# Kernel optimization log

Hardware: AMD Instinct MI355X
Metric: run time of the kernel (lower is better)

The kernel has to match this reference:

```python
import jax, jax.numpy as jnp
import numpy as np

B, N, FIN, FOUT = 32, 1024, 128, 128
NEG_SLOPE = 0.01  # torch nn.LeakyReLU default


def setup_inputs() -> dict:
    key = jax.random.key(0)
    k1, k2, k3, k4 = jax.random.split(key, 4)
    node_mat = jax.random.normal(k1, (B, N, FIN), dtype=jnp.float32)
    adj_mat = jax.random.uniform(k2, (B, N, N), dtype=jnp.float32)
    # nn.Linear(FIN, FOUT): weight [FOUT, FIN], bias [FOUT]
    bound = 1.0 / np.sqrt(FIN)
    W = jax.random.uniform(k3, (FOUT, FIN), minval=-bound, maxval=bound, dtype=jnp.float32)
    b = jax.random.uniform(k4, (FOUT,), minval=-bound, maxval=bound, dtype=jnp.float32)
    return {"node_mat": node_mat, "adj_mat": adj_mat, "W": W, "b": b}


def reference(node_mat, adj_mat, W, b):
    # degree per node: row-sum of adjacency [B, N, 1]
    n_neighbors = adj_mat.sum(axis=-1, keepdims=True)
    # D^-1 A : the original builds eye*(1/deg) then bmm; algebraically a row scaling
    norm_adj = adj_mat / n_neighbors                      # [B, N, N]
    agg = jnp.einsum('bnm,bmf->bnf', norm_adj, node_mat)  # [B, N, FIN]
    out = jnp.einsum('bnf,of->bno', agg, W) + b           # [B, N, FOUT]
    return jnp.where(out >= 0, out, NEG_SLOPE * out)      # LeakyReLU
```

## Files before the change

kernel.cpp:

```cpp
#include <hip/hip_runtime.h>
#include <cstdint>
#include <cstddef>

#define BB   32
#define NN   1024
#define FIN  128
#define FOUT 128

typedef __attribute__((ext_vector_type(8))) short bf16x8;
typedef __attribute__((ext_vector_type(4))) float f32x4;

__device__ __forceinline__ unsigned int f2bf(float f) {
    union { float f; unsigned int u; } v; v.f = f;
    unsigned int u = v.u;
    return (u + 0x7FFFu + ((u >> 16) & 1u)) >> 16;
}
__device__ __forceinline__ unsigned int pack2(float a, float b) {
    return f2bf(a) | (f2bf(b) << 16);
}

__global__ __launch_bounds__(256) void y_kernel(const float* __restrict__ node,
                                                const float* __restrict__ W,
                                                unsigned short* __restrict__ Yt) {
    __shared__ unsigned short Alds[64 * 136];
    __shared__ unsigned short Blds[128 * 136];

    const int tid = threadIdx.x;
    const int bid = blockIdx.x;
    const int b   = bid >> 4;
    const int m0  = (bid & 15) * 64;

    {
        const int r  = tid >> 2;
        const int c0 = (tid & 3) * 32;
        const float* src = node + ((size_t)b * NN + m0 + r) * FIN + c0;
        float4 v[8];
        #pragma unroll
        for (int j = 0; j < 8; ++j) v[j] = ((const float4*)src)[j];
        #pragma unroll
        for (int j = 0; j < 4; ++j) {
            uint4 p;
            p.x = pack2(v[2*j].x,   v[2*j].y);
            p.y = pack2(v[2*j].z,   v[2*j].w);
            p.z = pack2(v[2*j+1].x, v[2*j+1].y);
            p.w = pack2(v[2*j+1].z, v[2*j+1].w);
            *(uint4*)&Alds[r * 136 + c0 + j * 8] = p;
        }
    }
    {
        const int r  = tid >> 1;
        const int c0 = (tid & 1) * 64;
        const float* src = W + r * FIN + c0;
        #pragma unroll
        for (int j = 0; j < 8; ++j) {
            float4 v0 = ((const float4*)src)[2*j];
            float4 v1 = ((const float4*)src)[2*j + 1];
            uint4 p;
            p.x = pack2(v0.x, v0.y);
            p.y = pack2(v0.z, v0.w);
            p.z = pack2(v1.x, v1.y);
            p.w = pack2(v1.z, v1.w);
            *(uint4*)&Blds[r * 136 + c0 + j * 8] = p;
        }
    }
    __syncthreads();

    const int w = tid >> 6, lane = tid & 63;
    const int wm = (w & 1) * 32, wn = (w >> 1) * 64;
    const int lcol = lane & 15, lk = (lane >> 4) * 8;

    f32x4 acc[2][4] = {};
    #pragma unroll
    for (int kc = 0; kc < 4; ++kc) {
        const int kof = kc * 32 + lk;
        bf16x8 a[2], bb[4];
        #pragma unroll
        for (int mi = 0; mi < 2; ++mi)
            a[mi] = *(const bf16x8*)&Alds[(wm + mi*16 + lcol) * 136 + kof];
        #pragma unroll
        for (int ni = 0; ni < 4; ++ni)
            bb[ni] = *(const bf16x8*)&Blds[(wn + ni*16 + lcol) * 136 + kof];
        #pragma unroll
        for (int mi = 0; mi < 2; ++mi)
            #pragma unroll
            for (int ni = 0; ni < 4; ++ni)
                acc[mi][ni] = __builtin_amdgcn_mfma_f32_16x16x32_bf16(
                    a[mi], bb[ni], acc[mi][ni], 0, 0, 0);
    }
    __syncthreads();

    unsigned short* Clds = Blds;
    const int rq = (lane >> 4) * 4;
    #pragma unroll
    for (int mi = 0; mi < 2; ++mi) {
        const int mloc = wm + mi * 16 + rq;
        #pragma unroll
        for (int ni = 0; ni < 4; ++ni) {
            const int o = wn + ni * 16 + lcol;
            uint2 p;
            p.x = pack2(acc[mi][ni][0], acc[mi][ni][1]);
            p.y = pack2(acc[mi][ni][2], acc[mi][ni][3]);
            *(uint2*)&Clds[o * 72 + mloc] = p;
        }
    }
    __syncthreads();

    {
        const int o = tid >> 1, half = tid & 1;
        unsigned short* dst = Yt + ((size_t)b * FOUT + o) * NN + m0 + half * 32;
        const unsigned short* s = &Clds[o * 72 + half * 32];
        #pragma unroll
        for (int j = 0; j < 8; ++j) ((uint2*)dst)[j] = ((const uint2*)s)[j];
    }
}

__global__ __launch_bounds__(256) void gcn_kernel(const float* __restrict__ adj,
                                                  const unsigned short* __restrict__ Yt,
                                                  const float* __restrict__ bias,
                                                  float* __restrict__ out) {
    __shared__ unsigned short Alds[64 * 72];
    __shared__ unsigned short Blds[128 * 72];
    __shared__ float rs[64];

    const int tid = threadIdx.x;
    const int bid = blockIdx.x;
    const int b   = bid >> 4;
    const int n0  = (bid & 15) * 64;

    const int ar  = tid >> 2;
    const int ac0 = (tid & 3) * 16;
    const int br  = tid >> 1;
    const int bc0 = (tid & 1) * 32;

    const float*          aptr = adj + ((size_t)b * NN + n0 + ar) * NN + ac0;
    const unsigned short* bptr = Yt  + ((size_t)b * FOUT + br) * NN + bc0;

    float rsum = 0.f;
    float4 av[4];
    uint4  bv[4];
    #pragma unroll
    for (int j = 0; j < 4; ++j) av[j] = ((const float4*)aptr)[j];
    #pragma unroll
    for (int j = 0; j < 4; ++j) bv[j] = ((const uint4*)bptr)[j];

    const int w = tid >> 6, lane = tid & 63;
    const int wm = (w & 1) * 32, wn = (w >> 1) * 64;
    const int lcol = lane & 15, lk = (lane >> 4) * 8;

    f32x4 acc[2][4] = {};

    for (int s = 0; s < 16; ++s) {
        #pragma unroll
        for (int j = 0; j < 4; ++j) {
            float4 v = av[j];
            rsum += (v.x + v.y) + (v.z + v.w);
            uint2 p;
            p.x = pack2(v.x, v.y);
            p.y = pack2(v.z, v.w);
            *(uint2*)&Alds[ar * 72 + ac0 + j * 4] = p;
        }
        #pragma unroll
        for (int j = 0; j < 4; ++j)
            *(uint4*)&Blds[br * 72 + bc0 + j * 8] = bv[j];

        if (s < 15) {
            const float*          ap = aptr + (s + 1) * 64;
            const unsigned short* bp = bptr + (s + 1) * 64;
            #pragma unroll
            for (int j = 0; j < 4; ++j) av[j] = ((const float4*)ap)[j];
            #pragma unroll
            for (int j = 0; j < 4; ++j) bv[j] = ((const uint4*)bp)[j];
        }
        __syncthreads();

        #pragma unroll
        for (int kc = 0; kc < 2; ++kc) {
            const int kof = kc * 32 + lk;
            bf16x8 af[2], bf_[4];
            #pragma unroll
            for (int mi = 0; mi < 2; ++mi)
                af[mi] = *(const bf16x8*)&Alds[(wm + mi*16 + lcol) * 72 + kof];
            #pragma unroll
            for (int ni = 0; ni < 4; ++ni)
                bf_[ni] = *(const bf16x8*)&Blds[(wn + ni*16 + lcol) * 72 + kof];
            #pragma unroll
            for (int mi = 0; mi < 2; ++mi)
                #pragma unroll
                for (int ni = 0; ni < 4; ++ni)
                    acc[mi][ni] = __builtin_amdgcn_mfma_f32_16x16x32_bf16(
                        af[mi], bf_[ni], acc[mi][ni], 0, 0, 0);
        }
        __syncthreads();
    }

    rsum += __shfl_xor(rsum, 1);
    rsum += __shfl_xor(rsum, 2);
    if ((tid & 3) == 0) rs[ar] = rsum;
    __syncthreads();

    const int rq = (lane >> 4) * 4;
    float* outB = out + ((size_t)b * NN + n0) * FOUT;
    float bcol[4];
    #pragma unroll
    for (int ni = 0; ni < 4; ++ni) bcol[ni] = bias[wn + ni * 16 + lcol];

    #pragma unroll
    for (int mi = 0; mi < 2; ++mi) {
        const int rbase = wm + mi * 16 + rq;
        float sc[4];
        #pragma unroll
        for (int j = 0; j < 4; ++j) sc[j] = 1.0f / rs[rbase + j];
        #pragma unroll
        for (int ni = 0; ni < 4; ++ni) {
            const int col = wn + ni * 16 + lcol;
            #pragma unroll
            for (int j = 0; j < 4; ++j) {
                float v = acc[mi][ni][j] * sc[j] + bcol[ni];
                v = (v >= 0.f) ? v : 0.01f * v;
                outB[(size_t)(rbase + j) * FOUT + col] = v;
            }
        }
    }
}

extern "C" void kernel_launch(void* const* d_in, const int* in_sizes, int n_in,
                              void* d_out, int out_size, void* d_ws, size_t ws_size,
                              hipStream_t stream) {
    const float* node = (const float*)d_in[0];
    const float* adj  = (const float*)d_in[1];
    const float* W    = (const float*)d_in[2];
    const float* bias = (const float*)d_in[3];
    float* out = (float*)d_out;
    unsigned short* Yt = (unsigned short*)d_ws;

    hipLaunchKernelGGL(y_kernel,   dim3(512), dim3(256), 0, stream, node, W, Yt);
    hipLaunchKernelGGL(gcn_kernel, dim3(512), dim3(256), 0, stream, adj, Yt, bias, out);
}
```

Before: 262.7 us.

## Halve GCN row tile, double grid, stage output via LDS for coalesced stores

The aggregation kernel now uses 32-row tiles with 1024 blocks instead of 64-row tiles with 512 blocks. This gives more parallelism and occupancy (launch bounds request 4 blocks) on the memory-bound adjacency stream, at the cost of reading Y twice as often per batch. The epilogue writes results into LDS and then stores coalesced float4 rows. The Y kernel is reorganised with coalesced loads, swapped MFMA operands and wider global stores of the transposed bf16 output.

```diff
diff --git a/kernel.cpp b/kernel.cpp
--- a/kernel.cpp
+++ b/kernel.cpp
@@ -22,51 +22,39 @@
 __global__ __launch_bounds__(256) void y_kernel(const float* __restrict__ node,
                                                 const float* __restrict__ W,
                                                 unsigned short* __restrict__ Yt) {
-    __shared__ unsigned short Alds[64 * 136];
-    __shared__ unsigned short Blds[128 * 136];
+    __shared__ unsigned short Wlds[128 * 136];
+    __shared__ unsigned short Nlds[64 * 136];
 
     const int tid = threadIdx.x;
     const int bid = blockIdx.x;
     const int b   = bid >> 4;
     const int m0  = (bid & 15) * 64;
 
+    #pragma unroll
+    for (int i = 0; i < 16; ++i) {
+        const int idx = i * 256 + tid;
+        const int row = idx >> 5;
+        const int c   = (idx & 31) * 4;
+        float4 v = ((const float4*)W)[idx];
+        uint2 p; p.x = pack2(v.x, v.y); p.y = pack2(v.z, v.w);
+        *(uint2*)&Wlds[row * 136 + c] = p;
+    }
     {
-        const int r  = tid >> 2;
-        const int c0 = (tid & 3) * 32;
-        const float* src = node + ((size_t)b * NN + m0 + r) * FIN + c0;
-        float4 v[8];
-        #pragma unroll
-        for (int j = 0; j < 8; ++j) v[j] = ((const float4*)src)[j];
-        #pragma unroll
-        for (int j = 0; j < 4; ++j) {
-            uint4 p;
-            p.x = pack2(v[2*j].x,   v[2*j].y);
-            p.y = pack2(v[2*j].z,   v[2*j].w);
-            p.z = pack2(v[2*j+1].x, v[2*j+1].y);
-            p.w = pack2(v[2*j+1].z, v[2*j+1].w);
-            *(uint4*)&Alds[r * 136 + c0 + j * 8] = p;
-        }
-    }
-    {
-        const int r  = tid >> 1;
-        const int c0 = (tid & 1) * 64;
-        const float* src = W + r * FIN + c0;
-        #pragma unroll
-        for (int j = 0; j < 8; ++j) {
-            float4 v0 = ((const float4*)src)[2*j];
-            float4 v1 = ((const float4*)src)[2*j + 1];
-            uint4 p;
-            p.x = pack2(v0.x, v0.y);
-            p.y = pack2(v0.z, v0.w);
-            p.z = pack2(v1.x, v1.y);
-            p.w = pack2(v1.z, v1.w);
-            *(uint4*)&Blds[r * 136 + c0 + j * 8] = p;
+        const float* base = node + ((size_t)b * NN + m0) * FIN;
+        #pragma unroll
+        for (int i = 0; i < 8; ++i) {
+            const int idx = i * 256 + tid;
+            const int row = idx >> 5;
+            const int c   = (idx & 31) * 4;
+            float4 v = *(const float4*)(base + row * FIN + c);
+            uint2 p; p.x = pack2(v.x, v.y); p.y = pack2(v.z, v.w);
+            *(uint2*)&Nlds[row * 136 + c] = p;
         }
     }
     __syncthreads();
 
     const int w = tid >> 6, lane = tid & 63;
-    const int wm = (w & 1) * 32, wn = (w >> 1) * 64;
+    const int wo = w * 32;
     const int lcol = lane & 15, lk = (lane >> 4) * 8;
 
     f32x4 acc[2][4] = {};
@@ -76,10 +64,10 @@
         bf16x8 a[2], bb[4];
         #pragma unroll
         for (int mi = 0; mi < 2; ++mi)
-            a[mi] = *(const bf16x8*)&Alds[(wm + mi*16 + lcol) * 136 + kof];
+            a[mi] = *(const bf16x8*)&Wlds[(wo + mi*16 + lcol) * 136 + kof];
         #pragma unroll
         for (int ni = 0; ni < 4; ++ni)
-            bb[ni] = *(const bf16x8*)&Blds[(wn + ni*16 + lcol) * 136 + kof];
+            bb[ni] = *(const bf16x8*)&Nlds[(ni*16 + lcol) * 136 + kof];
         #pragma unroll
         for (int mi = 0; mi < 2; ++mi)
             #pragma unroll
@@ -89,136 +77,134 @@
     }
     __syncthreads();
 
-    unsigned short* Clds = Blds;
+    unsigned short* Ylds = Wlds;
     const int rq = (lane >> 4) * 4;
     #pragma unroll
-    for (int mi = 0; mi < 2; ++mi) {
-        const int mloc = wm + mi * 16 + rq;
-        #pragma unroll
-        for (int ni = 0; ni < 4; ++ni) {
-            const int o = wn + ni * 16 + lcol;
-            uint2 p;
-            p.x = pack2(acc[mi][ni][0], acc[mi][ni][1]);
-            p.y = pack2(acc[mi][ni][2], acc[mi][ni][3]);
-            *(uint2*)&Clds[o * 72 + mloc] = p;
-        }
-    }
+    for (int mi = 0; mi < 2; ++mi)
+        #pragma unroll
+        for (int ni = 0; ni < 4; ++ni)
+            #pragma unroll
+            for (int r = 0; r < 4; ++r) {
+                const int o = wo + mi * 16 + rq + r;
+                const int m = ni * 16 + lcol;
+                Ylds[o * 72 + m] = (unsigned short)f2bf(acc[mi][ni][r]);
+            }
     __syncthreads();
 
     {
-        const int o = tid >> 1, half = tid & 1;
-        unsigned short* dst = Yt + ((size_t)b * FOUT + o) * NN + m0 + half * 32;
-        const unsigned short* s = &Clds[o * 72 + half * 32];
-        #pragma unroll
-        for (int j = 0; j < 8; ++j) ((uint2*)dst)[j] = ((const uint2*)s)[j];
-    }
-}
-
-__global__ __launch_bounds__(256) void gcn_kernel(const float* __restrict__ adj,
-                                                  const unsigned short* __restrict__ Yt,
-                                                  const float* __restrict__ bias,
-                                                  float* __restrict__ out) {
-    __shared__ unsigned short Alds[64 * 72];
-    __shared__ unsigned short Blds[128 * 72];
-    __shared__ float rs[64];
+        const int oq = tid >> 3, c = (tid & 7) * 8;
+        #pragma unroll
+        for (int j = 0; j < 4; ++j) {
+            const int o = oq + 32 * j;
+            uint4 v = *(const uint4*)&Ylds[o * 72 + c];
+            *(uint4*)(Yt + ((size_t)b * FOUT + o) * NN + m0 + c) = v;
+        }
+    }
+}
+
+__global__ __launch_bounds__(256, 4) void gcn_kernel(const float* __restrict__ adj,
+                                                     const unsigned short* __restrict__ Yt,
+                                                     const float* __restrict__ bias,
+                                                     float* __restrict__ out) {
+    __shared__ char smem[23040];
+    unsigned short* Alds = (unsigned short*)smem;
+    unsigned short* Blds = (unsigned short*)(smem + 4608);
+    float* Clds = (float*)smem;
+    __shared__ float rs[32];
 
     const int tid = threadIdx.x;
     const int bid = blockIdx.x;
-    const int b   = bid >> 4;
-    const int n0  = (bid & 15) * 64;
-
-    const int ar  = tid >> 2;
-    const int ac0 = (tid & 3) * 16;
-    const int br  = tid >> 1;
-    const int bc0 = (tid & 1) * 32;
-
-    const float*          aptr = adj + ((size_t)b * NN + n0 + ar) * NN + ac0;
-    const unsigned short* bptr = Yt  + ((size_t)b * FOUT + br) * NN + bc0;
+    const int b   = bid >> 5;
+    const int n0  = (bid & 31) * 32;
+
+    const int arow = tid >> 3;
+    const int kq   = tid & 7;
+
+    const float*          aptr = adj + ((size_t)b * NN + n0 + arow) * NN + kq * 8;
+    const unsigned short* bptr = Yt  + ((size_t)b * FOUT + arow) * NN + kq * 8;
 
     float rsum = 0.f;
-    float4 av[4];
+    float4 av[2];
     uint4  bv[4];
     #pragma unroll
-    for (int j = 0; j < 4; ++j) av[j] = ((const float4*)aptr)[j];
-    #pragma unroll
-    for (int j = 0; j < 4; ++j) bv[j] = ((const uint4*)bptr)[j];
+    for (int j = 0; j < 2; ++j) av[j] = *(const float4*)(aptr + j * 4);
+    #pragma unroll
+    for (int j = 0; j < 4; ++j) bv[j] = *(const uint4*)(bptr + (size_t)j * 32 * NN);
 
     const int w = tid >> 6, lane = tid & 63;
-    const int wm = (w & 1) * 32, wn = (w >> 1) * 64;
+    const int wm = (w & 1) * 16, wn = (w >> 1) * 64;
     const int lcol = lane & 15, lk = (lane >> 4) * 8;
 
-    f32x4 acc[2][4] = {};
+    f32x4 acc[4] = {};
 
     for (int s = 0; s < 16; ++s) {
         #pragma unroll
-        for (int j = 0; j < 4; ++j) {
+        for (int j = 0; j < 2; ++j) {
             float4 v = av[j];
             rsum += (v.x + v.y) + (v.z + v.w);
-            uint2 p;
-            p.x = pack2(v.x, v.y);
-            p.y = pack2(v.z, v.w);
-            *(uint2*)&Alds[ar * 72 + ac0 + j * 4] = p;
+            uint2 p; p.x = pack2(v.x, v.y); p.y = pack2(v.z, v.w);
+            *(uint2*)&Alds[arow * 72 + kq * 8 + j * 4] = p;
         }
         #pragma unroll
         for (int j = 0; j < 4; ++j)
-            *(uint4*)&Blds[br * 72 + bc0 + j * 8] = bv[j];
+            *(uint4*)&Blds[(arow + 32 * j) * 72 + kq * 8] = bv[j];
 
         if (s < 15) {
             const float*          ap = aptr + (s + 1) * 64;
             const unsigned short* bp = bptr + (s + 1) * 64;
             #pragma unroll
-            for (int j = 0; j < 4; ++j) av[j] = ((const float4*)ap)[j];
-            #pragma unroll
-            for (int j = 0; j < 4; ++j) bv[j] = ((const uint4*)bp)[j];
+            for (int j = 0; j < 2; ++j) av[j] = *(const float4*)(ap + j * 4);
+            #pragma unroll
+            for (int j = 0; j < 4; ++j) bv[j] = *(const uint4*)(bp + (size_t)j * 32 * NN);
         }
         __syncthreads();
 
         #pragma unroll
         for (int kc = 0; kc < 2; ++kc) {
             const int kof = kc * 32 + lk;
-            bf16x8 af[2], bf_[4];
-            #pragma unroll
-            for (int mi = 0; mi < 2; ++mi)
-                af[mi] = *(const bf16x8*)&Alds[(wm + mi*16 + lcol) * 72 + kof];
+            bf16x8 af = *(const bf16x8*)&Alds[(wm + lcol) * 72 + kof];
+            bf16x8 bf_[4];
             #pragma unroll
             for (int ni = 0; ni < 4; ++ni)
                 bf_[ni] = *(const bf16x8*)&Blds[(wn + ni*16 + lcol) * 72 + kof];
             #pragma unroll
-            for (int mi = 0; mi < 2; ++mi)
-                #pragma unroll
-                for (int ni = 0; ni < 4; ++ni)
-                    acc[mi][ni] = __builtin_amdgcn_mfma_f32_16x16x32_bf16(
-                        af[mi], bf_[ni], acc[mi][ni], 0, 0, 0);
+            for (int ni = 0; ni < 4; ++ni)
+                acc[ni] = __builtin_amdgcn_mfma_f32_16x16x32_bf16(
+                    af, bf_[ni], acc[ni], 0, 0, 0);
         }
         __syncthreads();
     }
 
     rsum += __shfl_xor(rsum, 1);
     rsum += __shfl_xor(rsum, 2);
-    if ((tid & 3) == 0) rs[ar] = rsum;
+    rsum += __shfl_xor(rsum, 4);
+    if ((tid & 7) == 0) rs[arow] = rsum;
     __syncthreads();
 
     const int rq = (lane >> 4) * 4;
-    float* outB = out + ((size_t)b * NN + n0) * FOUT;
-    float bcol[4];
-    #pragma unroll
-    for (int ni = 0; ni < 4; ++ni) bcol[ni] = bias[wn + ni * 16 + lcol];
-
-    #pragma unroll
-    for (int mi = 0; mi < 2; ++mi) {
-        const int rbase = wm + mi * 16 + rq;
-        float sc[4];
-        #pragma unroll
-        for (int j = 0; j < 4; ++j) sc[j] = 1.0f / rs[rbase + j];
-        #pragma unroll
-        for (int ni = 0; ni < 4; ++ni) {
-            const int col = wn + ni * 16 + lcol;
-            #pragma unroll
-            for (int j = 0; j < 4; ++j) {
-                float v = acc[mi][ni][j] * sc[j] + bcol[ni];
-                v = (v >= 0.f) ? v : 0.01f * v;
-                outB[(size_t)(rbase + j) * FOUT + col] = v;
-            }
+    #pragma unroll
+    for (int ni = 0; ni < 4; ++ni) {
+        const int col = wn + ni * 16 + lcol;
+        const float bc = bias[col];
+        #pragma unroll
+        for (int r = 0; r < 4; ++r) {
+            const int row = wm + rq + r;
+            float v = acc[ni][r] * (1.0f / rs[row]) + bc;
+            v = (v >= 0.f) ? v : 0.01f * v;
+            Clds[row * 136 + col] = v;
+        }
+    }
+    __syncthreads();
+
+    {
+        float* outB = out + ((size_t)b * NN + n0) * FOUT;
+        #pragma unroll
+        for (int i = 0; i < 4; ++i) {
+            const int idx = i * 256 + tid;
+            const int row = idx >> 5;
+            const int c   = (idx & 31) * 4;
+            float4 v = *(const float4*)&Clds[row * 136 + c];
+            *(float4*)(outB + (size_t)row * FOUT + c) = v;
         }
     }
 }
@@ -233,6 +219,6 @@
     float* out = (float*)d_out;
     unsigned short* Yt = (unsigned short*)d_ws;
 
-    hipLaunchKernelGGL(y_kernel,   dim3(512), dim3(256), 0, stream, node, W, Yt);
-    hipLaunchKernelGGL(gcn_kernel, dim3(512), dim3(256), 0, stream, adj, Yt, bias, out);
-}
+    hipLaunchKernelGGL(y_kernel,   dim3(512),  dim3(256), 0, stream, node, W, Yt);
+    hipLaunchKernelGGL(gcn_kernel, dim3(1024), dim3(256), 0, stream, adj, Yt, bias, out);
+}
```

Result: slower. 290.1 us (+10.4%).
